# Performance work log

Hardware: AMD Instinct MI355X
Metric: run time of the kernel (lower is better)

The kernel has to match this reference:

```python
import jax, jax.numpy as jnp
import numpy as np

# QLSTMClassifier (quantum mode): Embedding -> QLSTM (4 quantum gate layers per step) -> Linear -> log_softmax.
# NOTE: QLSTM.forward unbinds dim 0 (batch) and cats each x:(seq,emb) with hx:(batch,hid),
# which requires batch == seq_len. We honor that with S = batch = seq_len.
S = 256   # batch == seq_len
E = 1024  # embedding_dim
H = 10    # hidden_dim == n_qubits (required by f*cx elementwise product)
V = 50257 # vocab_size
T = 50    # tagset_size


def setup_inputs() -> dict:
    key = jax.random.key(0)
    ks = jax.random.split(key, 6)
    sentence = jax.random.randint(ks[0], (S, S), 0, V)                                   # (batch, seq)
    emb_table = jax.random.normal(ks[1], (V, E), jnp.float32) * 0.02                      # nn.Embedding weight
    Wg = jax.random.normal(ks[2], (4, E + H, H), jnp.float32) * (1.0 / np.sqrt(E + H))    # forget/input/update/output linears
    bg = jnp.zeros((4, H), jnp.float32)
    theta = jax.random.normal(ks[3], (4, H), jnp.float32)                                 # trainable RX angles per gate
    W_out = jax.random.normal(ks[4], (H, T), jnp.float32) * (1.0 / np.sqrt(H))            # hidden2tag
    b_out = jnp.zeros((T,), jnp.float32)
    return dict(sentence=sentence, emb_table=emb_table, Wg=Wg, bg=bg,
                theta=theta, W_out=W_out, b_out=b_out)


def _qlayer(z, th):
    # Exact closed form of the QLayer circuit on n wires starting from |0...0>:
    #   RX(z_w) then RX(th_w) on wire w  ==> RX(a_w) with a_w = z_w + th_w (product state),
    #   then CNOT ring: CNOT(0,1), CNOT(1,2), ..., CNOT(n-2,n-1), CNOT(n-1,0),
    # Heisenberg-picture pullback of Z_w through the CNOT ring gives
    #   M_0 = Z_1 Z_2 ... Z_{n-1},   M_w = Z_0 Z_1 ... Z_w  (w >= 1),
    # and on the product state <Z_j> = cos(a_j), so expectations factorize:
    #   out_0 = prod_{j>=1} cos(a_j),  out_w = prod_{j<=w} cos(a_j).
    c = jnp.cos(z + th)                                   # (B, H)
    cum = jnp.cumprod(c, axis=-1)                         # prefix products
    tail = jnp.prod(c[:, 1:], axis=-1, keepdims=True)     # wire-0 observable
    return jnp.concatenate([tail, cum[:, 1:]], axis=-1)   # (B, H)


def reference(sentence, emb_table, Wg, bg, theta, W_out, b_out):
    embeds = emb_table[sentence]                          # (S, S, E); scan axis = dim 0 (unbind dim)
    h0 = jnp.zeros((embeds.shape[0], theta.shape[1]), embeds.dtype)

    def step(carry, x):                                   # x: (S, E)
        hx, cx = carry
        comb = jnp.concatenate([x, hx], axis=-1)          # (S, E+H)
        z = jnp.einsum('bi,gio->gbo', comb, Wg) + bg[:, None, :]  # (4, S, H)
        f = jax.nn.sigmoid(_qlayer(z[0], theta[0]))
        i = jax.nn.sigmoid(_qlayer(z[1], theta[1]))
        g = jnp.tanh(_qlayer(z[2], theta[2]))
        o = jax.nn.sigmoid(_qlayer(z[3], theta[3]))
        cx = f * cx + i * g
        hx = o * jnp.tanh(cx)
        return (hx, cx), hx

    _, outs = jax.lax.scan(step, (h0, h0), embeds)        # (S, S, H)
    logits = outs @ W_out + b_out                         # (S, S, T)
    return jax.nn.log_softmax(logits, axis=2)
```

## Files before the change

### kernel.cpp

```cpp
#include <hip/hip_runtime.h>
#include <hip/hip_bf16.h>


#define E_DIM 1024
#define H_DIM 10
#define NC 40
#define EHS 10340
#define KT 16
#define ALD_STRIDE 516

__global__ __launch_bounds__(256) void k_wt(const float* __restrict__ Wg,
                                            float* __restrict__ Wt) {
    int i = blockIdx.x * 256 + threadIdx.x;
    if (i < E_DIM * NC) {
        int k = i / NC, c = i % NC;
        int g = c / H_DIM, h = c % H_DIM;
        Wt[i] = Wg[g * EHS + k * H_DIM + h];
    }
}

__global__ __launch_bounds__(256, 2) void k_gemm(const int* __restrict__ idx,
                                                 const float* __restrict__ emb,
                                                 const float* __restrict__ Wt,
                                                 float* __restrict__ pre) {
    __shared__ float A_lds[KT * ALD_STRIDE];
    __shared__ float W_lds[KT * NC];

    const int tid = threadIdx.x;
    const int rb = blockIdx.x & 127;
    const int split = blockIdx.x >> 7;
    const int rowbase = rb * 512;
    const int k0 = split * 256;
    const int rt = tid >> 2;
    const int cg = tid & 3;
    const int r0 = rt * 8;
    const int c0 = cg * 10;

    int idx8[8];
#pragma unroll
    for (int it = 0; it < 8; ++it) idx8[it] = idx[rowbase + (tid >> 2) + it * 64];

    float acc[8][10];
#pragma unroll
    for (int r = 0; r < 8; ++r)
#pragma unroll
        for (int c = 0; c < 10; ++c) acc[r][c] = 0.0f;

    for (int kt = 0; kt < 256 / KT; ++kt) {
        const int ktb = k0 + kt * KT;
        __syncthreads();
        if (tid < 160) {
            float4 wv = *(const float4*)(Wt + (size_t)ktb * NC + tid * 4);
            *(float4*)&W_lds[tid * 4] = wv;
        }
#pragma unroll
        for (int it = 0; it < 8; ++it) {
            int row = (tid >> 2) + it * 64;
            const float* p = emb + (size_t)idx8[it] * E_DIM + ktb + (tid & 3) * 4;
            float4 v = *(const float4*)p;
            int kl = (tid & 3) * 4;
            A_lds[(kl + 0) * ALD_STRIDE + row] = v.x;
            A_lds[(kl + 1) * ALD_STRIDE + row] = v.y;
            A_lds[(kl + 2) * ALD_STRIDE + row] = v.z;
            A_lds[(kl + 3) * ALD_STRIDE + row] = v.w;
        }
        __syncthreads();
#pragma unroll 4
        for (int k = 0; k < KT; ++k) {
            float4 a0 = *(const float4*)&A_lds[k * ALD_STRIDE + r0];
            float4 a1 = *(const float4*)&A_lds[k * ALD_STRIDE + r0 + 4];
            float w[10];
#pragma unroll
            for (int i = 0; i < 5; ++i) {
                float2 wv = *(const float2*)&W_lds[k * NC + c0 + 2 * i];
                w[2 * i] = wv.x; w[2 * i + 1] = wv.y;
            }
            float ar[8] = {a0.x, a0.y, a0.z, a0.w, a1.x, a1.y, a1.z, a1.w};
#pragma unroll
            for (int r = 0; r < 8; ++r)
#pragma unroll
                for (int c = 0; c < 10; ++c)
                    acc[r][c] = fmaf(ar[r], w[c], acc[r][c]);
        }
    }
#pragma unroll
    for (int r = 0; r < 8; ++r) {
        size_t base = ((size_t)split * 65536 + rowbase + r0 + r) * NC + c0;
#pragma unroll
        for (int i = 0; i < 5; ++i) {
            float2 st = {acc[r][2 * i], acc[r][2 * i + 1]};
            *(float2*)&pre[base + 2 * i] = st;
        }
    }
}

template <int CTRL>
__device__ __forceinline__ float dpp1(float x) {
    return __int_as_float(__builtin_amdgcn_update_dpp(
        __float_as_int(1.0f), __float_as_int(x), CTRL, 0xF, 0xF, false));
}
#define ROW_SHR(n) (0x110 + (n))
#define ROW_SHL(n) (0x100 + (n))

__global__ __launch_bounds__(64) void k_rnn(const float* __restrict__ pre,
                                            const float* __restrict__ Wg,
                                            const float* __restrict__ bg,
                                            const float* __restrict__ theta,
                                            float* __restrict__ outs) {
    const int lane = threadIdx.x;
    const int b = blockIdx.x;
    const int r = lane >> 4;
    const int h = lane & 15;
    const int hc = (h < 10) ? h : 9;
    const int c = r * 10 + hc;

    float Wh[10];
#pragma unroll
    for (int j = 0; j < 10; ++j) Wh[j] = Wg[r * EHS + (E_DIM + j) * H_DIM + hc];
    const float bias = bg[c] + theta[c];

    const float kk = (r == 2) ? 2.0f : -1.0f;
    const float aa = (r == 2) ? 1.0f : 0.0f;
    const float bb = (r == 2) ? -2.0f : 1.0f;

    const size_t pstride = (size_t)65536 * NC;
    const float* p = pre + (size_t)b * NC + c;
    float z0 = p[0], z1 = p[pstride], z2 = p[2 * pstride], z3 = p[3 * pstride];
    float cx = 0.0f, hx = 0.0f;

    for (int t = 0; t < 256; ++t) {
        int tn = (t + 1 < 256) ? t + 1 : 255;
        const float* pn = pre + ((size_t)tn * 256 + b) * NC + c;
        float n0 = pn[0], n1 = pn[pstride], n2 = pn[2 * pstride], n3 = pn[3 * pstride];

        float hv0 = __shfl(hx, 0), hv1 = __shfl(hx, 1), hv2 = __shfl(hx, 2),
              hv3 = __shfl(hx, 3), hv4 = __shfl(hx, 4), hv5 = __shfl(hx, 5),
              hv6 = __shfl(hx, 6), hv7 = __shfl(hx, 7), hv8 = __shfl(hx, 8),
              hv9 = __shfl(hx, 9);
        float d0 = fmaf(hv0, Wh[0], fmaf(hv2, Wh[2],
                   fmaf(hv4, Wh[4], fmaf(hv6, Wh[6], hv8 * Wh[8]))));
        float d1 = fmaf(hv1, Wh[1], fmaf(hv3, Wh[3],
                   fmaf(hv5, Wh[5], fmaf(hv7, Wh[7], hv9 * Wh[9]))));
        float z = ((z0 + z1) + (z2 + z3)) + bias + (d0 + d1);

        float cc = __builtin_amdgcn_cosf(z * 0.15915494309189535f);

        float pp = cc;
        pp *= dpp1<ROW_SHR(1)>(pp);
        pp *= dpp1<ROW_SHR(2)>(pp);
        pp *= dpp1<ROW_SHR(4)>(pp);
        pp *= dpp1<ROW_SHR(8)>(pp);
        float ss = (h < 10) ? cc : 1.0f;
        ss *= dpp1<ROW_SHL(1)>(ss);
        ss *= dpp1<ROW_SHL(2)>(ss);
        ss *= dpp1<ROW_SHL(4)>(ss);
        ss *= dpp1<ROW_SHL(8)>(ss);
        float tl = dpp1<ROW_SHL(1)>(ss);
        float q = (h == 0) ? tl : pp;

        float e = __expf(kk * q);
        float act = fmaf(bb, __builtin_amdgcn_rcpf(1.0f + e), aa);

        float fv = __shfl(act, h);
        float iv = __shfl(act, 16 + h);
        float gv = __shfl(act, 32 + h);
        float ov = __shfl(act, 48 + h);

        cx = fmaf(fv, cx, iv * gv);
        float e2 = __expf(2.0f * cx);
        float th = fmaf(-2.0f, __builtin_amdgcn_rcpf(1.0f + e2), 1.0f);
        hx = ov * th;

        if (lane < 10) outs[((size_t)t * 256 + b) * H_DIM + lane] = hx;

        z0 = n0; z1 = n1; z2 = n2; z3 = n3;
    }
}

__global__ __launch_bounds__(256) void k_head(const float* __restrict__ outs,
                                              const float* __restrict__ Wo,
                                              const float* __restrict__ bo,
                                              float* __restrict__ out) {
    const size_t row = blockIdx.x * 256 + threadIdx.x;
    float hx[10];
#pragma unroll
    for (int i = 0; i < 5; ++i) {
        float2 v = *(const float2*)&outs[row * H_DIM + 2 * i];
        hx[2 * i] = v.x; hx[2 * i + 1] = v.y;
    }
    float lg[50];
#pragma unroll
    for (int cI = 0; cI < 50; ++cI) {
        float l = bo[cI];
#pragma unroll
        for (int j = 0; j < 10; ++j) l = fmaf(hx[j], Wo[j * 50 + cI], l);
        lg[cI] = l;
    }
    float m = lg[0];
#pragma unroll
    for (int cI = 1; cI < 50; ++cI) m = fmaxf(m, lg[cI]);
    float sum = 0.0f;
#pragma unroll
    for (int cI = 0; cI < 50; ++cI) sum += __expf(lg[cI] - m);
    float lse = m + __logf(sum);
#pragma unroll
    for (int i = 0; i < 25; ++i) {
        float2 v = {lg[2 * i] - lse, lg[2 * i + 1] - lse};
        *(float2*)&out[row * 50 + 2 * i] = v;
    }
}

extern "C" void kernel_launch(void* const* d_in, const int* in_sizes, int n_in,
                              void* d_out, int out_size, void* d_ws, size_t ws_size,
                              hipStream_t stream) {
    const int*   sentence = (const int*)d_in[0];
    const float* emb      = (const float*)d_in[1];
    const float* Wg       = (const float*)d_in[2];
    const float* bg       = (const float*)d_in[3];
    const float* theta    = (const float*)d_in[4];
    const float* Wo       = (const float*)d_in[5];
    const float* bo       = (const float*)d_in[6];
    float* out = (float*)d_out;

    float* ws   = (float*)d_ws;
    float* Wt   = ws;
    float* pre  = ws + 40960;
    float* outs = pre + (size_t)4 * 65536 * NC;

    k_wt<<<160, 256, 0, stream>>>(Wg, Wt);
    k_gemm<<<512, 256, 0, stream>>>(sentence, emb, Wt, pre);
    k_rnn<<<256, 64, 0, stream>>>(pre, Wg, bg, theta, outs);
    k_head<<<256, 256, 0, stream>>>(outs, Wo, bo, out);
}
```

Measured before the change: 451.9 us.

## Prefetch GEMM tiles into registers, shrink tiles, transpose z layout for RNN prefetch

```diff
diff --git a/kernel.cpp b/kernel.cpp
--- a/kernel.cpp
+++ b/kernel.cpp
@@ -7,7 +7,7 @@
 #define NC 40
 #define EHS 10340
 #define KT 16
-#define ALD_STRIDE 516
+#define ALD 260
 
 __global__ __launch_bounds__(256) void k_wt(const float* __restrict__ Wg,
                                             float* __restrict__ Wt) {
@@ -19,77 +19,87 @@
     }
 }
 
-__global__ __launch_bounds__(256, 2) void k_gemm(const int* __restrict__ idx,
+__global__ __launch_bounds__(256, 4) void k_gemm(const int* __restrict__ idx,
                                                  const float* __restrict__ emb,
                                                  const float* __restrict__ Wt,
-                                                 float* __restrict__ pre) {
-    __shared__ float A_lds[KT * ALD_STRIDE];
+                                                 float* __restrict__ zs) {
+    __shared__ float A_lds[KT * ALD];
     __shared__ float W_lds[KT * NC];
 
     const int tid = threadIdx.x;
-    const int rb = blockIdx.x & 127;
-    const int split = blockIdx.x >> 7;
-    const int rowbase = rb * 512;
+    const int rb = blockIdx.x & 255;
+    const int split = blockIdx.x >> 8;
+    const int rowbase = rb * 256;
     const int k0 = split * 256;
     const int rt = tid >> 2;
     const int cg = tid & 3;
-    const int r0 = rt * 8;
+    const int r0 = rt * 4;
     const int c0 = cg * 10;
-
-    int idx8[8];
-#pragma unroll
-    for (int it = 0; it < 8; ++it) idx8[it] = idx[rowbase + (tid >> 2) + it * 64];
-
-    float acc[8][10];
-#pragma unroll
-    for (int r = 0; r < 8; ++r)
+    const int kl = cg * 4;
+
+    const float* aptr[4];
+#pragma unroll
+    for (int it = 0; it < 4; ++it) {
+        int gi = idx[rowbase + rt + it * 64];
+        aptr[it] = emb + (size_t)gi * E_DIM + k0 + kl;
+    }
+
+    float acc[4][10];
+#pragma unroll
+    for (int r = 0; r < 4; ++r)
 #pragma unroll
         for (int c = 0; c < 10; ++c) acc[r][c] = 0.0f;
 
+    float4 v[4];
+#pragma unroll
+    for (int it = 0; it < 4; ++it) v[it] = *(const float4*)aptr[it];
+    float4 wv;
+    if (tid < 160) wv = *(const float4*)(Wt + (size_t)k0 * NC + tid * 4);
+
     for (int kt = 0; kt < 256 / KT; ++kt) {
-        const int ktb = k0 + kt * KT;
         __syncthreads();
-        if (tid < 160) {
-            float4 wv = *(const float4*)(Wt + (size_t)ktb * NC + tid * 4);
-            *(float4*)&W_lds[tid * 4] = wv;
-        }
-#pragma unroll
-        for (int it = 0; it < 8; ++it) {
-            int row = (tid >> 2) + it * 64;
-            const float* p = emb + (size_t)idx8[it] * E_DIM + ktb + (tid & 3) * 4;
-            float4 v = *(const float4*)p;
-            int kl = (tid & 3) * 4;
-            A_lds[(kl + 0) * ALD_STRIDE + row] = v.x;
-            A_lds[(kl + 1) * ALD_STRIDE + row] = v.y;
-            A_lds[(kl + 2) * ALD_STRIDE + row] = v.z;
-            A_lds[(kl + 3) * ALD_STRIDE + row] = v.w;
-        }
+#pragma unroll
+        for (int it = 0; it < 4; ++it) {
+            int row = rt + it * 64;
+            A_lds[(kl + 0) * ALD + row] = v[it].x;
+            A_lds[(kl + 1) * ALD + row] = v[it].y;
+            A_lds[(kl + 2) * ALD + row] = v[it].z;
+            A_lds[(kl + 3) * ALD + row] = v[it].w;
+        }
+        if (tid < 160) *(float4*)&W_lds[tid * 4] = wv;
         __syncthreads();
+        if (kt < 15) {
+#pragma unroll
+            for (int it = 0; it < 4; ++it)
+                v[it] = *(const float4*)(aptr[it] + (kt + 1) * KT);
+            if (tid < 160)
+                wv = *(const float4*)(Wt + (size_t)(k0 + (kt + 1) * KT) * NC + tid * 4);
+        }
 #pragma unroll 4
         for (int k = 0; k < KT; ++k) {
-            float4 a0 = *(const float4*)&A_lds[k * ALD_STRIDE + r0];
-            float4 a1 = *(const float4*)&A_lds[k * ALD_STRIDE + r0 + 4];
+            float4 a = *(const float4*)&A_lds[k * ALD + r0];
             float w[10];
 #pragma unroll
             for (int i = 0; i < 5; ++i) {
-                float2 wv = *(const float2*)&W_lds[k * NC + c0 + 2 * i];
-                w[2 * i] = wv.x; w[2 * i + 1] = wv.y;
+                float2 t2 = *(const float2*)&W_lds[k * NC + c0 + 2 * i];
+                w[2 * i] = t2.x; w[2 * i + 1] = t2.y;
             }
-            float ar[8] = {a0.x, a0.y, a0.z, a0.w, a1.x, a1.y, a1.z, a1.w};
-#pragma unroll
-            for (int r = 0; r < 8; ++r)
+            float ar[4] = {a.x, a.y, a.z, a.w};
+#pragma unroll
+            for (int r = 0; r < 4; ++r)
 #pragma unroll
                 for (int c = 0; c < 10; ++c)
                     acc[r][c] = fmaf(ar[r], w[c], acc[r][c]);
         }
     }
 #pragma unroll
-    for (int r = 0; r < 8; ++r) {
-        size_t base = ((size_t)split * 65536 + rowbase + r0 + r) * NC + c0;
+    for (int r = 0; r < 4; ++r) {
+        int b = r0 + r;
+        size_t base = ((size_t)(split * 256 + b) * 256 + rb) * NC + c0;
 #pragma unroll
         for (int i = 0; i < 5; ++i) {
             float2 st = {acc[r][2 * i], acc[r][2 * i + 1]};
-            *(float2*)&pre[base + 2 * i] = st;
+            *(float2*)&zs[base + 2 * i] = st;
         }
     }
 }
@@ -102,7 +112,7 @@
 #define ROW_SHR(n) (0x110 + (n))
 #define ROW_SHL(n) (0x100 + (n))
 
-__global__ __launch_bounds__(64) void k_rnn(const float* __restrict__ pre,
+__global__ __launch_bounds__(64) void k_rnn(const float* __restrict__ zs,
                                             const float* __restrict__ Wg,
                                             const float* __restrict__ bg,
                                             const float* __restrict__ theta,
@@ -123,15 +133,30 @@
     const float aa = (r == 2) ? 1.0f : 0.0f;
     const float bb = (r == 2) ? -2.0f : 1.0f;
 
-    const size_t pstride = (size_t)65536 * NC;
-    const float* p = pre + (size_t)b * NC + c;
-    float z0 = p[0], z1 = p[pstride], z2 = p[2 * pstride], z3 = p[3 * pstride];
+    const size_t sstr = (size_t)256 * 256 * NC;
+    const float* p0 = zs + (size_t)b * 256 * NC + c;
+    const float* p1 = p0 + sstr;
+    const float* p2 = p0 + 2 * sstr;
+    const float* p3 = p0 + 3 * sstr;
+
+    float a0[4], a1[4], a2[4], a3[4];
+#pragma unroll
+    for (int u = 0; u < 4; ++u) {
+        a0[u] = p0[u * NC]; a1[u] = p1[u * NC];
+        a2[u] = p2[u * NC]; a3[u] = p3[u * NC];
+    }
+
     float cx = 0.0f, hx = 0.0f;
 
+#pragma unroll 4
     for (int t = 0; t < 256; ++t) {
-        int tn = (t + 1 < 256) ? t + 1 : 255;
-        const float* pn = pre + ((size_t)tn * 256 + b) * NC + c;
-        float n0 = pn[0], n1 = pn[pstride], n2 = pn[2 * pstride], n3 = pn[3 * pstride];
+        const int u = t & 3;
+        float z40 = ((a0[u] + a1[u]) + (a2[u] + a3[u])) + bias;
+        {
+            int tn = (t + 4 < 256) ? t + 4 : 255;
+            a0[u] = p0[tn * NC]; a1[u] = p1[tn * NC];
+            a2[u] = p2[tn * NC]; a3[u] = p3[tn * NC];
+        }
 
         float hv0 = __shfl(hx, 0), hv1 = __shfl(hx, 1), hv2 = __shfl(hx, 2),
               hv3 = __shfl(hx, 3), hv4 = __shfl(hx, 4), hv5 = __shfl(hx, 5),
@@ -141,7 +166,7 @@
                    fmaf(hv4, Wh[4], fmaf(hv6, Wh[6], hv8 * Wh[8]))));
         float d1 = fmaf(hv1, Wh[1], fmaf(hv3, Wh[3],
                    fmaf(hv5, Wh[5], fmaf(hv7, Wh[7], hv9 * Wh[9]))));
-        float z = ((z0 + z1) + (z2 + z3)) + bias + (d0 + d1);
+        float z = z40 + (d0 + d1);
 
         float cc = __builtin_amdgcn_cosf(z * 0.15915494309189535f);
 
@@ -172,8 +197,6 @@
         hx = ov * th;
 
         if (lane < 10) outs[((size_t)t * 256 + b) * H_DIM + lane] = hx;
-
-        z0 = n0; z1 = n1; z2 = n2; z3 = n3;
     }
 }
 
@@ -224,11 +247,11 @@
 
     float* ws   = (float*)d_ws;
     float* Wt   = ws;
-    float* pre  = ws + 40960;
-    float* outs = pre + (size_t)4 * 65536 * NC;
+    float* zs   = ws + 40960;
+    float* outs = zs + (size_t)4 * 65536 * NC;
 
     k_wt<<<160, 256, 0, stream>>>(Wg, Wt);
-    k_gemm<<<512, 256, 0, stream>>>(sentence, emb, Wt, pre);
-    k_rnn<<<256, 64, 0, stream>>>(pre, Wg, bg, theta, outs);
+    k_gemm<<<1024, 256, 0, stream>>>(sentence, emb, Wt, zs);
+    k_rnn<<<256, 64, 0, stream>>>(zs, Wg, bg, theta, outs);
     k_head<<<256, 256, 0, stream>>>(outs, Wo, bo, out);
 }
```

Measured after the change: 404.9 us. -10.4%, faster.

## Use bf16 MFMA for gate projection and stage RNN inputs via LDS producer wave

Applied to the files above, without the earlier changes.

```diff
diff --git a/kernel.cpp b/kernel.cpp
--- a/kernel.cpp
+++ b/kernel.cpp
@@ -6,91 +6,81 @@
 #define H_DIM 10
 #define NC 40
 #define EHS 10340
-#define KT 16
-#define ALD_STRIDE 516
+
+typedef __attribute__((ext_vector_type(8))) short bf16x8;
+typedef __attribute__((ext_vector_type(4))) float f32x4;
+
+__device__ __forceinline__ unsigned short f2bf(float f) {
+    unsigned u = __float_as_uint(f);
+    unsigned r = u + 0x7FFFu + ((u >> 16) & 1u);
+    return (unsigned short)(r >> 16);
+}
 
 __global__ __launch_bounds__(256) void k_wt(const float* __restrict__ Wg,
-                                            float* __restrict__ Wt) {
+                                            unsigned short* __restrict__ Bfg) {
     int i = blockIdx.x * 256 + threadIdx.x;
-    if (i < E_DIM * NC) {
-        int k = i / NC, c = i % NC;
-        int g = c / H_DIM, h = c % H_DIM;
-        Wt[i] = Wg[g * EHS + k * H_DIM + h];
-    }
-}
-
-__global__ __launch_bounds__(256, 2) void k_gemm(const int* __restrict__ idx,
+    if (i >= 6144) return;
+    int lane = i & 63, nt = (i >> 6) % 3, c = i / 192;
+    int kg = lane >> 4, n = lane & 15;
+    int nc = nt * 16 + n;
+    unsigned short v[8];
+#pragma unroll
+    for (int j = 0; j < 8; ++j) {
+        int k = c * 32 + kg * 8 + j;
+        float w = 0.0f;
+        if (nc < NC) {
+            int g = nc / H_DIM, h = nc % H_DIM;
+            w = Wg[g * EHS + k * H_DIM + h];
+        }
+        v[j] = f2bf(w);
+    }
+    bf16x8* dst = (bf16x8*)(Bfg + (size_t)i * 8);
+    bf16x8 pk;
+#pragma unroll
+    for (int j = 0; j < 8; ++j) pk[j] = (short)v[j];
+    *dst = pk;
+}
+
+__global__ __launch_bounds__(256, 4) void k_gemm(const int* __restrict__ idx,
                                                  const float* __restrict__ emb,
-                                                 const float* __restrict__ Wt,
-                                                 float* __restrict__ pre) {
-    __shared__ float A_lds[KT * ALD_STRIDE];
-    __shared__ float W_lds[KT * NC];
-
+                                                 const unsigned short* __restrict__ Bfg,
+                                                 float* __restrict__ zs) {
     const int tid = threadIdx.x;
-    const int rb = blockIdx.x & 127;
-    const int split = blockIdx.x >> 7;
-    const int rowbase = rb * 512;
-    const int k0 = split * 256;
-    const int rt = tid >> 2;
-    const int cg = tid & 3;
-    const int r0 = rt * 8;
-    const int c0 = cg * 10;
-
-    int idx8[8];
-#pragma unroll
-    for (int it = 0; it < 8; ++it) idx8[it] = idx[rowbase + (tid >> 2) + it * 64];
-
-    float acc[8][10];
-#pragma unroll
-    for (int r = 0; r < 8; ++r)
-#pragma unroll
-        for (int c = 0; c < 10; ++c) acc[r][c] = 0.0f;
-
-    for (int kt = 0; kt < 256 / KT; ++kt) {
-        const int ktb = k0 + kt * KT;
-        __syncthreads();
-        if (tid < 160) {
-            float4 wv = *(const float4*)(Wt + (size_t)ktb * NC + tid * 4);
-            *(float4*)&W_lds[tid * 4] = wv;
-        }
-#pragma unroll
-        for (int it = 0; it < 8; ++it) {
-            int row = (tid >> 2) + it * 64;
-            const float* p = emb + (size_t)idx8[it] * E_DIM + ktb + (tid & 3) * 4;
-            float4 v = *(const float4*)p;
-            int kl = (tid & 3) * 4;
-            A_lds[(kl + 0) * ALD_STRIDE + row] = v.x;
-            A_lds[(kl + 1) * ALD_STRIDE + row] = v.y;
-            A_lds[(kl + 2) * ALD_STRIDE + row] = v.z;
-            A_lds[(kl + 3) * ALD_STRIDE + row] = v.w;
-        }
-        __syncthreads();
-#pragma unroll 4
-        for (int k = 0; k < KT; ++k) {
-            float4 a0 = *(const float4*)&A_lds[k * ALD_STRIDE + r0];
-            float4 a1 = *(const float4*)&A_lds[k * ALD_STRIDE + r0 + 4];
-            float w[10];
-#pragma unroll
-            for (int i = 0; i < 5; ++i) {
-                float2 wv = *(const float2*)&W_lds[k * NC + c0 + 2 * i];
-                w[2 * i] = wv.x; w[2 * i + 1] = wv.y;
-            }
-            float ar[8] = {a0.x, a0.y, a0.z, a0.w, a1.x, a1.y, a1.z, a1.w};
-#pragma unroll
-            for (int r = 0; r < 8; ++r)
-#pragma unroll
-                for (int c = 0; c < 10; ++c)
-                    acc[r][c] = fmaf(ar[r], w[c], acc[r][c]);
-        }
-    }
-#pragma unroll
-    for (int r = 0; r < 8; ++r) {
-        size_t base = ((size_t)split * 65536 + rowbase + r0 + r) * NC + c0;
-#pragma unroll
-        for (int i = 0; i < 5; ++i) {
-            float2 st = {acc[r][2 * i], acc[r][2 * i + 1]};
-            *(float2*)&pre[base + 2 * i] = st;
-        }
+    const int wave = tid >> 6, lane = tid & 63;
+    const int R0 = (blockIdx.x * 4 + wave) * 16;
+    const int m = lane & 15, q = lane >> 4;
+
+    const int token = idx[R0 + m];
+    const float* arow = emb + (size_t)token * E_DIM + q * 8;
+
+    f32x4 acc0 = {0.f, 0.f, 0.f, 0.f}, acc1 = acc0, acc2 = acc0;
+
+#pragma unroll 2
+    for (int c = 0; c < 32; ++c) {
+        float4 a0 = *(const float4*)(arow + c * 32);
+        float4 a1 = *(const float4*)(arow + c * 32 + 4);
+        bf16x8 b0 = *(const bf16x8*)(Bfg + ((size_t)(c * 3 + 0) * 64 + lane) * 8);
+        bf16x8 b1 = *(const bf16x8*)(Bfg + ((size_t)(c * 3 + 1) * 64 + lane) * 8);
+        bf16x8 b2 = *(const bf16x8*)(Bfg + ((size_t)(c * 3 + 2) * 64 + lane) * 8);
+        bf16x8 af;
+        af[0] = (short)f2bf(a0.x); af[1] = (short)f2bf(a0.y);
+        af[2] = (short)f2bf(a0.z); af[3] = (short)f2bf(a0.w);
+        af[4] = (short)f2bf(a1.x); af[5] = (short)f2bf(a1.y);
+        af[6] = (short)f2bf(a1.z); af[7] = (short)f2bf(a1.w);
+        acc0 = __builtin_amdgcn_mfma_f32_16x16x32_bf16(af, b0, acc0, 0, 0, 0);
+        acc1 = __builtin_amdgcn_mfma_f32_16x16x32_bf16(af, b1, acc1, 0, 0, 0);
+        acc2 = __builtin_amdgcn_mfma_f32_16x16x32_bf16(af, b2, acc2, 0, 0, 0);
+    }
+
+    const int t = R0 >> 8;
+    const int bbase = (R0 & 255) + q * 4;
+#pragma unroll
+    for (int i = 0; i < 4; ++i) {
+        int b = bbase + i;
+        size_t o = ((size_t)b * 256 + t) * NC;
+        zs[o + m] = acc0[i];
+        zs[o + 16 + m] = acc1[i];
+        if (m < 8) zs[o + 32 + m] = acc2[i];
     }
 }
 
@@ -102,78 +92,106 @@
 #define ROW_SHR(n) (0x110 + (n))
 #define ROW_SHL(n) (0x100 + (n))
 
-__global__ __launch_bounds__(64) void k_rnn(const float* __restrict__ pre,
-                                            const float* __restrict__ Wg,
-                                            const float* __restrict__ bg,
-                                            const float* __restrict__ theta,
-                                            float* __restrict__ outs) {
-    const int lane = threadIdx.x;
+__device__ __forceinline__ float rdlane(float v, int l) {
+    return __int_as_float(__builtin_amdgcn_readlane(__float_as_int(v), l));
+}
+
+__global__ __launch_bounds__(128) void k_rnn(const float* __restrict__ zs,
+                                             const float* __restrict__ Wg,
+                                             const float* __restrict__ bg,
+                                             const float* __restrict__ theta,
+                                             float* __restrict__ outs) {
+    __shared__ float zbuf[2][640];
+    const int tid = threadIdx.x;
     const int b = blockIdx.x;
-    const int r = lane >> 4;
-    const int h = lane & 15;
-    const int hc = (h < 10) ? h : 9;
-    const int c = r * 10 + hc;
-
-    float Wh[10];
-#pragma unroll
-    for (int j = 0; j < 10; ++j) Wh[j] = Wg[r * EHS + (E_DIM + j) * H_DIM + hc];
-    const float bias = bg[c] + theta[c];
-
-    const float kk = (r == 2) ? 2.0f : -1.0f;
-    const float aa = (r == 2) ? 1.0f : 0.0f;
-    const float bb = (r == 2) ? -2.0f : 1.0f;
-
-    const size_t pstride = (size_t)65536 * NC;
-    const float* p = pre + (size_t)b * NC + c;
-    float z0 = p[0], z1 = p[pstride], z2 = p[2 * pstride], z3 = p[3 * pstride];
-    float cx = 0.0f, hx = 0.0f;
-
-    for (int t = 0; t < 256; ++t) {
-        int tn = (t + 1 < 256) ? t + 1 : 255;
-        const float* pn = pre + ((size_t)tn * 256 + b) * NC + c;
-        float n0 = pn[0], n1 = pn[pstride], n2 = pn[2 * pstride], n3 = pn[3 * pstride];
-
-        float hv0 = __shfl(hx, 0), hv1 = __shfl(hx, 1), hv2 = __shfl(hx, 2),
-              hv3 = __shfl(hx, 3), hv4 = __shfl(hx, 4), hv5 = __shfl(hx, 5),
-              hv6 = __shfl(hx, 6), hv7 = __shfl(hx, 7), hv8 = __shfl(hx, 8),
-              hv9 = __shfl(hx, 9);
-        float d0 = fmaf(hv0, Wh[0], fmaf(hv2, Wh[2],
-                   fmaf(hv4, Wh[4], fmaf(hv6, Wh[6], hv8 * Wh[8]))));
-        float d1 = fmaf(hv1, Wh[1], fmaf(hv3, Wh[3],
-                   fmaf(hv5, Wh[5], fmaf(hv7, Wh[7], hv9 * Wh[9]))));
-        float z = ((z0 + z1) + (z2 + z3)) + bias + (d0 + d1);
-
-        float cc = __builtin_amdgcn_cosf(z * 0.15915494309189535f);
-
-        float pp = cc;
-        pp *= dpp1<ROW_SHR(1)>(pp);
-        pp *= dpp1<ROW_SHR(2)>(pp);
-        pp *= dpp1<ROW_SHR(4)>(pp);
-        pp *= dpp1<ROW_SHR(8)>(pp);
-        float ss = (h < 10) ? cc : 1.0f;
-        ss *= dpp1<ROW_SHL(1)>(ss);
-        ss *= dpp1<ROW_SHL(2)>(ss);
-        ss *= dpp1<ROW_SHL(4)>(ss);
-        ss *= dpp1<ROW_SHL(8)>(ss);
-        float tl = dpp1<ROW_SHL(1)>(ss);
-        float q = (h == 0) ? tl : pp;
-
-        float e = __expf(kk * q);
-        float act = fmaf(bb, __builtin_amdgcn_rcpf(1.0f + e), aa);
-
-        float fv = __shfl(act, h);
-        float iv = __shfl(act, 16 + h);
-        float gv = __shfl(act, 32 + h);
-        float ov = __shfl(act, 48 + h);
-
-        cx = fmaf(fv, cx, iv * gv);
-        float e2 = __expf(2.0f * cx);
-        float th = fmaf(-2.0f, __builtin_amdgcn_rcpf(1.0f + e2), 1.0f);
-        hx = ov * th;
-
-        if (lane < 10) outs[((size_t)t * 256 + b) * H_DIM + lane] = hx;
-
-        z0 = n0; z1 = n1; z2 = n2; z3 = n3;
+
+    if (tid >= 64) {
+        const int p = tid - 64;
+        const float* src = zs + (size_t)b * 256 * NC;
+#pragma unroll
+        for (int k = 0; k < 10; ++k) zbuf[0][p + k * 64] = src[p + k * 64];
+        __syncthreads();
+        for (int blk = 0; blk < 16; ++blk) {
+            if (blk + 1 < 16) {
+                const float* s2 = src + (blk + 1) * 640;
+                float v[10];
+#pragma unroll
+                for (int k = 0; k < 10; ++k) v[k] = s2[p + k * 64];
+#pragma unroll
+                for (int k = 0; k < 10; ++k) zbuf[(blk + 1) & 1][p + k * 64] = v[k];
+            }
+            __syncthreads();
+        }
+    } else {
+        const int lane = tid;
+        const int r = lane >> 4;
+        const int h = lane & 15;
+        const int hc = (h < 10) ? h : 9;
+        const int cidx = r * 10 + hc;
+
+        float Wh[10];
+#pragma unroll
+        for (int j = 0; j < 10; ++j) Wh[j] = Wg[r * EHS + (E_DIM + j) * H_DIM + hc];
+        const float bias = bg[cidx] + theta[cidx];
+
+        const float kk = (r == 2) ? 2.0f : -1.0f;
+        const float aa = (r == 2) ? 1.0f : 0.0f;
+        const float bb = (r == 2) ? -2.0f : 1.0f;
+
+        float cx = 0.0f, hx = 0.0f;
+        __syncthreads();
+
+        for (int blk = 0; blk < 16; ++blk) {
+            const float* zb = zbuf[blk & 1];
+            float zv = zb[cidx];
+#pragma unroll 4
+            for (int s = 0; s < 16; ++s) {
+                float znext = zb[((s < 15) ? (s + 1) * 40 : s * 40) + cidx];
+
+                float hv0 = rdlane(hx, 0), hv1 = rdlane(hx, 1), hv2 = rdlane(hx, 2),
+                      hv3 = rdlane(hx, 3), hv4 = rdlane(hx, 4), hv5 = rdlane(hx, 5),
+                      hv6 = rdlane(hx, 6), hv7 = rdlane(hx, 7), hv8 = rdlane(hx, 8),
+                      hv9 = rdlane(hx, 9);
+                float d0 = fmaf(hv0, Wh[0], fmaf(hv2, Wh[2],
+                           fmaf(hv4, Wh[4], fmaf(hv6, Wh[6], hv8 * Wh[8]))));
+                float d1 = fmaf(hv1, Wh[1], fmaf(hv3, Wh[3],
+                           fmaf(hv5, Wh[5], fmaf(hv7, Wh[7], hv9 * Wh[9]))));
+                float z = (zv + bias) + (d0 + d1);
+
+                float cc = __builtin_amdgcn_cosf(z * 0.15915494309189535f);
+
+                float pp = cc;
+                pp *= dpp1<ROW_SHR(1)>(pp);
+                pp *= dpp1<ROW_SHR(2)>(pp);
+                pp *= dpp1<ROW_SHR(4)>(pp);
+                pp *= dpp1<ROW_SHR(8)>(pp);
+                float ss = (h < 10) ? cc : 1.0f;
+                ss *= dpp1<ROW_SHL(1)>(ss);
+                ss *= dpp1<ROW_SHL(2)>(ss);
+                ss *= dpp1<ROW_SHL(4)>(ss);
+                ss *= dpp1<ROW_SHL(8)>(ss);
+                float tl = dpp1<ROW_SHL(1)>(ss);
+                float qv = (h == 0) ? tl : pp;
+
+                float e = __expf(kk * qv);
+                float act = fmaf(bb, __builtin_amdgcn_rcpf(1.0f + e), aa);
+
+                float fv = __shfl(act, h);
+                float iv = __shfl(act, 16 + h);
+                float gv = __shfl(act, 32 + h);
+                float ov = __shfl(act, 48 + h);
+
+                cx = fmaf(fv, cx, iv * gv);
+                float e2 = __expf(2.0f * cx);
+                float th = fmaf(-2.0f, __builtin_amdgcn_rcpf(1.0f + e2), 1.0f);
+                hx = ov * th;
+
+                int t = blk * 16 + s;
+                if (lane < 10) outs[((size_t)t * 256 + b) * H_DIM + lane] = hx;
+                zv = znext;
+            }
+            __syncthreads();
+        }
     }
 }
 
@@ -222,13 +240,13 @@
     const float* bo       = (const float*)d_in[6];
     float* out = (float*)d_out;
 
-    float* ws   = (float*)d_ws;
-    float* Wt   = ws;
-    float* pre  = ws + 40960;
-    float* outs = pre + (size_t)4 * 65536 * NC;
-
-    k_wt<<<160, 256, 0, stream>>>(Wg, Wt);
-    k_gemm<<<512, 256, 0, stream>>>(sentence, emb, Wt, pre);
-    k_rnn<<<256, 64, 0, stream>>>(pre, Wg, bg, theta, outs);
+    float* ws = (float*)d_ws;
+    unsigned short* Bfg = (unsigned short*)ws;
+    float* zs   = ws + 24576;
+    float* outs = zs + (size_t)256 * 256 * NC;
+
+    k_wt<<<24, 256, 0, stream>>>(Wg, Bfg);
+    k_gemm<<<1024, 256, 0, stream>>>(sentence, emb, Bfg, zs);
+    k_rnn<<<256, 128, 0, stream>>>(zs, Wg, bg, theta, outs);
     k_head<<<256, 256, 0, stream>>>(outs, Wo, bo, out);
 }
```

Result: faster. 382.6 us (-15.3%).
